# Kernel optimization log

Hardware: AMD Instinct MI355X
Metric: run time of the kernel (lower is better)

Reference implementation:

```python
import jax, jax.numpy as jnp
import numpy as np


def fps(xyz, npoint):
    # Farthest point sampling. xyz: [B, N, 3] -> idx [B, npoint] int32
    B, N, _ = xyz.shape
    d0 = jnp.full((B, N), 1e10, xyz.dtype)
    far0 = jnp.zeros((B,), jnp.int32)

    def step(carry, _):
        dist, far = carry
        centroid = jnp.take_along_axis(xyz, far[:, None, None], axis=1)  # [B,1,3]
        d = jnp.sum((xyz - centroid) ** 2, axis=-1)                      # [B,N]
        dist = jnp.minimum(dist, d)
        nxt = jnp.argmax(dist, axis=-1).astype(jnp.int32)
        return (dist, nxt), far

    _, idx = jax.lax.scan(step, (d0, far0), None, length=npoint)
    return idx.T  # [B, npoint]


def ball_query(radius, nsample, xyz, new_xyz):
    # xyz [B,N,3], new_xyz [B,S,3] -> idx [B,S,nsample] int32
    N = xyz.shape[1]
    sqr = (jnp.sum(new_xyz ** 2, -1)[:, :, None]
           + jnp.sum(xyz ** 2, -1)[:, None, :]
           - 2.0 * jnp.einsum('bsd,bnd->bsn', new_xyz, xyz))  # [B,S,N]
    idx = jnp.broadcast_to(jnp.arange(N, dtype=jnp.int32), sqr.shape)
    idx = jnp.where(sqr > radius * radius, N, idx)
    idx = jnp.sort(idx, axis=-1)[..., :nsample]
    first = idx[..., :1]  # centers are in xyz, so at least one in-radius index exists
    return jnp.where(idx == N, first, idx)


def _gather(x, idx):
    # x [B,N,C], idx [B,S,K] -> [B,S,K,C]
    return jax.vmap(lambda xb, ib: xb[ib])(x, idx)


def set_abstraction(xyz, points, npoint, radius, nsample, layers):
    # xyz [B,N,3]; points [B,N,D] or None; layers: list of (W [Co,Ci], b [Co])
    fps_idx = fps(xyz, npoint)                                   # [B,S]
    new_xyz = jnp.take_along_axis(xyz, fps_idx[..., None], axis=1)  # [B,S,3]
    idx = ball_query(radius, nsample, xyz, new_xyz)              # [B,S,K]
    grouped = _gather(xyz, idx) - new_xyz[:, :, None, :]         # [B,S,K,3] centered
    if points is not None:
        grouped = jnp.concatenate([grouped, _gather(points, idx)], axis=-1)
    feats = grouped  # [B,S,K,Cin]
    for W, b in layers:  # shared 1x1 conv MLP (BN folded, eval mode) + ReLU
        feats = jax.nn.relu(jnp.einsum('bskc,oc->bsko', feats, W) + b)
    new_points = jnp.max(feats, axis=2)  # max-pool over neighborhood -> [B,S,Cout]
    return new_xyz, new_points.transpose(0, 2, 1)  # [B,S,3], [B,Cout,S]


def setup_inputs() -> dict:
    key = jax.random.key(0)
    ks = jax.random.split(key, 13)
    xyz = jax.random.uniform(ks[0], (8, 6, 32768), dtype=jnp.float32)
    dims1 = [(64, 6), (64, 64), (128, 64)]
    dims2 = [(128, 131), (128, 128), (285, 128)]
    inp = {'xyz': xyz}
    i = 1
    for pre, dims in (('sa1', dims1), ('sa2', dims2)):
        for j, (o, c) in enumerate(dims, 1):
            inp[f'{pre}_w{j}'] = jax.random.normal(ks[i], (o, c), jnp.float32) * (1.0 / np.sqrt(c))
            inp[f'{pre}_b{j}'] = jax.random.normal(ks[i + 6], (o,), jnp.float32) * 0.05
            i += 1
    return inp


def reference(xyz, sa1_w1, sa1_b1, sa1_w2, sa1_b2, sa1_w3, sa1_b3,
              sa2_w1, sa2_b1, sa2_w2, sa2_b2, sa2_w3, sa2_b3):
    norm = xyz[:, 3:, :].transpose(0, 2, 1)   # [B,N,3]
    xyz3 = xyz[:, :3, :].transpose(0, 2, 1)   # [B,N,3]
    l1_xyz, l1_points = set_abstraction(
        xyz3, norm, 512, 0.025, 32,
        [(sa1_w1, sa1_b1), (sa1_w2, sa1_b2), (sa1_w3, sa1_b3)])
    l2_xyz, l2_points = set_abstraction(
        l1_xyz, l1_points.transpose(0, 2, 1), 256, 0.05, 64,
        [(sa2_w1, sa2_b1), (sa2_w2, sa2_b2), (sa2_w3, sa2_b3)])
    return l2_xyz.transpose(0, 2, 1), l2_points.transpose(0, 2, 1)  # [B,3,256],[B,256,285]
```

## Files before the change

### kernel.cpp

```cpp
#include <hip/hip_runtime.h>

#define N1 32768
#define NP1 512
#define NS1 32
#define N2 512
#define NP2 256
#define NS2 64
#define POISON 0xAAAAAAAAu

__device__ __forceinline__ float fadd(float a, float b){ return __fadd_rn(a,b); }
__device__ __forceinline__ float fmul(float a, float b){ return __fmul_rn(a,b); }
__device__ __forceinline__ float fsub(float a, float b){ return __fsub_rn(a,b); }

__device__ __forceinline__ float dist3(float px,float py,float pz,float cx,float cy,float cz){
    float dx = fsub(px,cx), dy = fsub(py,cy), dz = fsub(pz,cz);
    return fadd(fadd(fmul(dx,dx), fmul(dy,dy)), fmul(dz,dz));
}
__device__ __forceinline__ float sumsq3(float x,float y,float z){
    return fadd(fadd(fmul(x,x), fmul(y,y)), fmul(z,z));
}
__device__ __forceinline__ float dot3(float ax,float ay,float az,float bx,float by,float bz){
    return fadd(fadd(fmul(ax,bx), fmul(ay,by)), fmul(az,bz));
}

__device__ __forceinline__ unsigned long long shflmax64(unsigned long long k, int off){
    unsigned long long o = __shfl_xor(k, off, 64);
    return o > k ? o : k;
}

#define FPS1_M  16
#define ST1_X   (FPS1_M + NP1/4 + 1)

__global__ __launch_bounds__(256) void stage1_kernel(const float* __restrict__ xyz,
                                                     float* __restrict__ new_xyz1,
                                                     unsigned long long* __restrict__ bests,
                                                     int* __restrict__ idx1, float r2,
                                                     float* __restrict__ new_xyz2,
                                                     float* __restrict__ out0)
{
    const int x = blockIdx.x;
    const int b = blockIdx.y;
    const int t = threadIdx.x;
    const int lane = t & 63;
    const int wid  = t >> 6;
    const float* xb = xyz + (size_t)b * 6 * N1;

    if (x < FPS1_M) {
        const int m = x;
        __shared__ unsigned long long wb[4];
        __shared__ float cw[4];

        const int base = m * (N1 / FPS1_M);
        float px[8], py[8], pz[8], dd[8];
#pragma unroll
        for (int j = 0; j < 8; ++j) {
            int n = base + t + j * 256;
            px[j] = xb[n];
            py[j] = xb[N1 + n];
            pz[j] = xb[2*N1 + n];
            dd[j] = 1e10f;
        }

        float cx = xb[0], cy = xb[N1], cz = xb[2*N1];

        for (int s = 0; s < NP1; ++s) {
            if (m == 0 && t == 0) {
                unsigned* o = (unsigned*)(new_xyz1 + ((size_t)b*NP1 + s)*3);
                __hip_atomic_store(o+0, __float_as_uint(cx), __ATOMIC_RELAXED, __HIP_MEMORY_SCOPE_AGENT);
                __hip_atomic_store(o+1, __float_as_uint(cy), __ATOMIC_RELAXED, __HIP_MEMORY_SCOPE_AGENT);
                __hip_atomic_store(o+2, __float_as_uint(cz), __ATOMIC_RELAXED, __HIP_MEMORY_SCOPE_AGENT);
            }
            if (s == NP1 - 1) break;

            float bv = -1.0f; int bi = base + t;
#pragma unroll
            for (int j = 0; j < 8; ++j) {
                float d  = dist3(px[j],py[j],pz[j],cx,cy,cz);
                float nd = fminf(dd[j], d);
                dd[j] = nd;
                if (nd > bv) { bv = nd; bi = base + t + j*256; }
            }
            unsigned long long pk = ((unsigned long long)__float_as_uint(bv) << 15)
                                  | (unsigned long long)(32767 - bi);
            pk = shflmax64(pk, 1);  pk = shflmax64(pk, 2);  pk = shflmax64(pk, 4);
            pk = shflmax64(pk, 8);  pk = shflmax64(pk, 16); pk = shflmax64(pk, 32);
            if (lane == 0) wb[wid] = pk;
            __syncthreads();

            if (wid == 0) {
                unsigned long long k4 = (lane < 4) ? wb[lane] : 0ull;
                k4 = shflmax64(k4, 1); k4 = shflmax64(k4, 2);
                unsigned long long* slotPar = bests + ((size_t)b*2 + (s & 1))*FPS1_M;
                if (lane == 0)
                    __hip_atomic_store(slotPar + m, (k4 << 10) | (unsigned long long)s,
                                       __ATOMIC_RELAXED, __HIP_MEMORY_SCOPE_AGENT);
                unsigned long long myv = 0; bool done = (lane >= FPS1_M);
                float ccx = 0.f, ccy = 0.f, ccz = 0.f;
                while (__ballot(done) != 0xFFFFFFFFFFFFFFFFull) {
                    if (!done) {
                        unsigned long long v = __hip_atomic_load(slotPar + lane,
                                                 __ATOMIC_RELAXED, __HIP_MEMORY_SCOPE_AGENT);
                        if ((unsigned)(v & 1023ull) == (unsigned)s) {
                            done = true; myv = v;
                            int idx = 32767 - (int)((v >> 10) & 0x7fffull);
                            ccx = xb[idx]; ccy = xb[N1 + idx]; ccz = xb[2*N1 + idx];
                        }
                    }
                }
                unsigned long long w = myv;
                w = shflmax64(w, 1); w = shflmax64(w, 2); w = shflmax64(w, 4); w = shflmax64(w, 8);
                int wl = (int)__ffsll(__ballot(myv == w)) - 1;
                float ncx = __shfl(ccx, wl, 64);
                float ncy = __shfl(ccy, wl, 64);
                float ncz = __shfl(ccz, wl, 64);
                if (lane == 0) { cw[0] = ncx; cw[1] = ncy; cw[2] = ncz; }
            }
            __syncthreads();
            cx = cw[0]; cy = cw[1]; cz = cw[2];
        }
        return;
    }

    if (x < FPS1_M + NP1/4) {
        const int s = (x - FPS1_M)*4 + wid;
        unsigned ux = 0, uy = 0, uz = 0;
        if (lane == 0) {
            const unsigned* cp = (const unsigned*)(new_xyz1 + ((size_t)b*NP1 + s)*3);
            for (;;) {
                ux = __hip_atomic_load(cp+0, __ATOMIC_RELAXED, __HIP_MEMORY_SCOPE_AGENT);
                uy = __hip_atomic_load(cp+1, __ATOMIC_RELAXED, __HIP_MEMORY_SCOPE_AGENT);
                uz = __hip_atomic_load(cp+2, __ATOMIC_RELAXED, __HIP_MEMORY_SCOPE_AGENT);
                if (ux != POISON && uy != POISON && uz != POISON) break;
                __builtin_amdgcn_s_sleep(32);
            }
        }
        float cx = __uint_as_float(__shfl((int)ux, 0, 64));
        float cy = __uint_as_float(__shfl((int)uy, 0, 64));
        float cz = __uint_as_float(__shfl((int)uz, 0, 64));

        float snew = sumsq3(cx,cy,cz);
        int* out = idx1 + ((size_t)b*NP1 + s)*NS1;
        int cnt = 0, first = 0;
        for (int ch = 0; ch < N1/64; ++ch) {
            int n = ch*64 + lane;
            float px_ = xb[n], py_ = xb[N1+n], pz_ = xb[2*N1+n];
            float sx  = sumsq3(px_,py_,pz_);
            float dt  = dot3(cx,cy,cz,px_,py_,pz_);
            float sqr = fsub(fadd(snew, sx), fmul(2.0f, dt));
            bool inb = !(sqr > r2);
            unsigned long long mask = __ballot(inb);
            if (mask) {
                if (cnt == 0) first = ch*64 + (int)(__ffsll((unsigned long long)mask) - 1);
                if (inb) {
                    int pos = cnt + (int)__popcll(mask & ((1ull << lane) - 1ull));
                    if (pos < NS1) out[pos] = n;
                }
                cnt += (int)__popcll(mask);
                if (cnt >= NS1) break;
            }
        }
        int c = cnt < NS1 ? cnt : NS1;
        if (lane < NS1 && lane >= c) out[lane] = first;
        return;
    }

    {
        __shared__ float c3[N2*3];
        const float* src = new_xyz1 + (size_t)b*N2*3;
        for (int e = t; e < N2*3; e += 256) {
            const unsigned* sp = (const unsigned*)(src + e);
            unsigned v;
            for (;;) {
                v = __hip_atomic_load(sp, __ATOMIC_RELAXED, __HIP_MEMORY_SCOPE_AGENT);
                if (v != POISON) break;
                __builtin_amdgcn_s_sleep(32);
            }
            c3[e] = __uint_as_float(v);
        }
        __syncthreads();
        if (t >= 64) return;

        float px[8], py[8], pz[8], dd[8];
#pragma unroll
        for (int j = 0; j < 8; ++j) {
            int n = t + j*64;
            px[j] = c3[n*3]; py[j] = c3[n*3+1]; pz[j] = c3[n*3+2];
            dd[j] = 1e10f;
        }
        int cur = 0;
        for (int s = 0; s < NP2; ++s) {
            float cx = c3[cur*3], cy = c3[cur*3+1], cz = c3[cur*3+2];
            if (t == 0) {
                float* o = new_xyz2 + ((size_t)b*NP2 + s)*3;
                o[0]=cx; o[1]=cy; o[2]=cz;
                out0[b*3*NP2 + s]         = cx;
                out0[b*3*NP2 + NP2 + s]   = cy;
                out0[b*3*NP2 + 2*NP2 + s] = cz;
            }
            float bv = -1.0f; int bi = 0;
#pragma unroll
            for (int j = 0; j < 8; ++j) {
                float d  = dist3(px[j],py[j],pz[j],cx,cy,cz);
                float nd = fminf(dd[j], d);
                dd[j] = nd;
                int n = t + j*64;
                if (nd > bv) { bv = nd; bi = n; }
            }
            unsigned long long pk = ((unsigned long long)__float_as_uint(bv) << 9)
                                  | (unsigned long long)(511 - bi);
            pk = shflmax64(pk, 1);  pk = shflmax64(pk, 2);  pk = shflmax64(pk, 4);
            pk = shflmax64(pk, 8);  pk = shflmax64(pk, 16); pk = shflmax64(pk, 32);
            cur = 511 - (int)(pk & 511ull);
        }
    }
}

__global__ __launch_bounds__(256) void mlp1_ball2_kernel(const float* __restrict__ xyz,
    const float* __restrict__ new_xyz1, const int* __restrict__ idx1,
    const float* __restrict__ W1, const float* __restrict__ B1,
    const float* __restrict__ W2, const float* __restrict__ B2,
    const float* __restrict__ W3, const float* __restrict__ B3,
    float* __restrict__ l1_points,
    const float* __restrict__ new_xyz2, int* __restrict__ idx2, float r2b)
{
    const int b = blockIdx.y;
    const int t = threadIdx.x;

    if (blockIdx.x >= NP1) {
        if (t < 64) {
            const int s = blockIdx.x - NP1;
            const int lane = t;
            const float* pb = new_xyz1 + (size_t)b*N2*3;
            const float* cp = new_xyz2 + ((size_t)b*NP2 + s)*3;
            float cx = cp[0], cy = cp[1], cz = cp[2];
            float snew = sumsq3(cx,cy,cz);
            int* out = idx2 + ((size_t)b*NP2 + s)*NS2;
            int cnt = 0, first = 0;
            for (int ch = 0; ch < N2/64; ++ch) {
                int n = ch*64 + lane;
                float x = pb[n*3], y = pb[n*3+1], z = pb[n*3+2];
                float sx  = sumsq3(x,y,z);
                float dt  = dot3(cx,cy,cz,x,y,z);
                float sqr = fsub(fadd(snew, sx), fmul(2.0f, dt));
                bool inb = !(sqr > r2b);
                unsigned long long mask = __ballot(inb);
                if (mask) {
                    if (cnt == 0) first = ch*64 + (int)(__ffsll((unsigned long long)mask) - 1);
                    if (inb) {
                        int pos = cnt + (int)__popcll(mask & ((1ull << lane) - 1ull));
                        if (pos < NS2) out[pos] = n;
                    }
                    cnt += (int)__popcll(mask);
                    if (cnt >= NS2) break;
                }
            }
            int c = cnt < NS2 ? cnt : NS2;
            if (lane >= c) out[lane] = first;
        }
        return;
    }

    const int s = blockIdx.x;
    const float* xb = xyz + (size_t)b*6*N1;
    __shared__ __align__(16) float inb_[NS1][6];
    __shared__ __align__(16) float h1_[NS1][64];
    __shared__ __align__(16) float h2_[NS1][64];
    __shared__ __align__(16) float red_[2][128];
    __shared__ int sidx[NS1];

    const float* cp = new_xyz1 + ((size_t)b*NP1 + s)*3;
    float c0 = cp[0], c1 = cp[1], c2 = cp[2];
    if (t < NS1) sidx[t] = idx1[((size_t)b*NP1+s)*NS1 + t];
    __syncthreads();
    if (t < NS1*6) {
        int k = t / 6, c = t % 6;
        int n = sidx[k];
        float v = xb[(size_t)c*N1 + n];
        if (c == 0) v -= c0; else if (c == 1) v -= c1; else if (c == 2) v -= c2;
        inb_[k][c] = v;
    }
    __syncthreads();
    {
        int o = t & 63, kg = t >> 6;
        float w[6];
#pragma unroll
        for (int c = 0; c < 6; ++c) w[c] = W1[o*6+c];
        float bias = B1[o];
#pragma unroll
        for (int kk = 0; kk < 8; ++kk) {
            int k = kg*8 + kk;
            float a = 0.f;
#pragma unroll
            for (int c = 0; c < 6; ++c) a = fmaf(inb_[k][c], w[c], a);
            h1_[k][o] = fmaxf(a + bias, 0.f);
        }
    }
    __syncthreads();
    {
        int o = t & 63, kg = t >> 6;
        float acc[8] = {};
        for (int ch = 0; ch < 8; ++ch) {
            const float4 wa = *(const float4*)&W2[o*64 + ch*8];
            const float4 wbv = *(const float4*)&W2[o*64 + ch*8 + 4];
#pragma unroll
            for (int kk = 0; kk < 8; ++kk) {
                int k = kg*8+kk;
                const float4 a0 = *(const float4*)&h1_[k][ch*8];
                const float4 a1 = *(const float4*)&h1_[k][ch*8+4];
                acc[kk] = fmaf(a0.x, wa.x, acc[kk]);
                acc[kk] = fmaf(a0.y, wa.y, acc[kk]);
                acc[kk] = fmaf(a0.z, wa.z, acc[kk]);
                acc[kk] = fmaf(a0.w, wa.w, acc[kk]);
                acc[kk] = fmaf(a1.x, wbv.x, acc[kk]);
                acc[kk] = fmaf(a1.y, wbv.y, acc[kk]);
                acc[kk] = fmaf(a1.z, wbv.z, acc[kk]);
                acc[kk] = fmaf(a1.w, wbv.w, acc[kk]);
            }
        }
        float bias = B2[o];
#pragma unroll
        for (int kk = 0; kk < 8; ++kk) h2_[kg*8+kk][o] = fmaxf(acc[kk] + bias, 0.f);
    }
    __syncthreads();
    {
        int o = t & 127, kg = t >> 7;
        float acc[16] = {};
        for (int ch = 0; ch < 8; ++ch) {
            const float4 wa = *(const float4*)&W3[o*64 + ch*8];
            const float4 wbv = *(const float4*)&W3[o*64 + ch*8 + 4];
#pragma unroll
            for (int kk = 0; kk < 16; ++kk) {
                int k = kg*16+kk;
                const float4 a0 = *(const float4*)&h2_[k][ch*8];
                const float4 a1 = *(const float4*)&h2_[k][ch*8+4];
                acc[kk] = fmaf(a0.x, wa.x, acc[kk]);
                acc[kk] = fmaf(a0.y, wa.y, acc[kk]);
                acc[kk] = fmaf(a0.z, wa.z, acc[kk]);
                acc[kk] = fmaf(a0.w, wa.w, acc[kk]);
                acc[kk] = fmaf(a1.x, wbv.x, acc[kk]);
                acc[kk] = fmaf(a1.y, wbv.y, acc[kk]);
                acc[kk] = fmaf(a1.z, wbv.z, acc[kk]);
                acc[kk] = fmaf(a1.w, wbv.w, acc[kk]);
            }
        }
        float bias = B3[o];
        float m = -1e30f;
#pragma unroll
        for (int kk = 0; kk < 16; ++kk) m = fmaxf(m, fmaxf(acc[kk] + bias, 0.f));
        red_[kg][o] = m;
    }
    __syncthreads();
    if (t < 128) {
        float m = fmaxf(red_[0][t], red_[1][t]);
        l1_points[((size_t)b*NP1+s)*128 + t] = m;
    }
}

__global__ __launch_bounds__(256) void mlp2_kernel(
    const float* __restrict__ new_xyz1, const float* __restrict__ l1_points,
    const float* __restrict__ new_xyz2, const int* __restrict__ idx2,
    const float* __restrict__ W1, const float* __restrict__ B1,
    const float* __restrict__ W2, const float* __restrict__ B2,
    const float* __restrict__ W3, const float* __restrict__ B3,
    float* __restrict__ out1)
{
    const int s = blockIdx.x, b = blockIdx.y;
    const int t = threadIdx.x;
    __shared__ __align__(16) float inb_[32][132];
    __shared__ __align__(16) float h1_[32][128];
    __shared__ __align__(16) float h2_[32][128];
    __shared__ int sidx[NS2];

    const float* cp = new_xyz2 + ((size_t)b*NP2+s)*3;
    float c0=cp[0], c1=cp[1], c2=cp[2];
    if (t < NS2) sidx[t] = idx2[((size_t)b*NP2+s)*NS2 + t];

    const int o1 = t & 63, o2 = o1 + 64, g = t >> 6;
    float vmax0 = -1e30f, vmax1 = -1e30f;

    for (int half = 0; half < 2; ++half) {
        __syncthreads();
        for (int e = t; e < 32*32; e += 256) {
            int kk = e >> 5, c4 = e & 31;
            int n = sidx[half*32 + kk];
            *(float4*)&inb_[kk][c4*4] =
                *(const float4*)&l1_points[((size_t)b*N2 + n)*128 + c4*4];
        }
        for (int e = t; e < 32*3; e += 256) {
            int kk = e / 3, c = e % 3;
            int n = sidx[half*32 + kk];
            inb_[kk][128 + c] = new_xyz1[((size_t)b*N2 + n)*3 + c]
                              - (c==0 ? c0 : (c==1 ? c1 : c2));
        }
        __syncthreads();
        {
            float accA[8] = {}, accB[8] = {};
            for (int ch = 0; ch < 16; ++ch) {
                float wa[8], wbv[8];
#pragma unroll
                for (int j = 0; j < 8; ++j) {
                    wa[j]  = W1[o1*131 + 3 + ch*8 + j];
                    wbv[j] = W1[o2*131 + 3 + ch*8 + j];
                }
#pragma unroll
                for (int kk = 0; kk < 8; ++kk) {
                    int k = g*8 + kk;
                    const float4 a0 = *(const float4*)&inb_[k][ch*8];
                    const float4 a1 = *(const float4*)&inb_[k][ch*8+4];
                    accA[kk] = fmaf(a0.x, wa[0], accA[kk]);
                    accA[kk] = fmaf(a0.y, wa[1], accA[kk]);
                    accA[kk] = fmaf(a0.z, wa[2], accA[kk]);
                    accA[kk] = fmaf(a0.w, wa[3], accA[kk]);
                    accA[kk] = fmaf(a1.x, wa[4], accA[kk]);
                    accA[kk] = fmaf(a1.y, wa[5], accA[kk]);
                    accA[kk] = fmaf(a1.z, wa[6], accA[kk]);
                    accA[kk] = fmaf(a1.w, wa[7], accA[kk]);
                    accB[kk] = fmaf(a0.x, wbv[0], accB[kk]);
                    accB[kk] = fmaf(a0.y, wbv[1], accB[kk]);
                    accB[kk] = fmaf(a0.z, wbv[2], accB[kk]);
                    accB[kk] = fmaf(a0.w, wbv[3], accB[kk]);
                    accB[kk] = fmaf(a1.x, wbv[4], accB[kk]);
                    accB[kk] = fmaf(a1.y, wbv[5], accB[kk]);
                    accB[kk] = fmaf(a1.z, wbv[6], accB[kk]);
                    accB[kk] = fmaf(a1.w, wbv[7], accB[kk]);
                }
            }
            float ta0=W1[o1*131+0], ta1=W1[o1*131+1], ta2=W1[o1*131+2];
            float tb0=W1[o2*131+0], tb1=W1[o2*131+1], tb2=W1[o2*131+2];
            float biasA = B1[o1], biasB = B1[o2];
#pragma unroll
            for (int kk = 0; kk < 8; ++kk) {
                int k = g*8 + kk;
                float f0 = inb_[k][128], f1 = inb_[k][129], f2 = inb_[k][130];
                float vA = accA[kk];
                vA = fmaf(f0, ta0, vA); vA = fmaf(f1, ta1, vA); vA = fmaf(f2, ta2, vA);
                float vB = accB[kk];
                vB = fmaf(f0, tb0, vB); vB = fmaf(f1, tb1, vB); vB = fmaf(f2, tb2, vB);
                h1_[k][o1] = fmaxf(vA + biasA, 0.f);
                h1_[k][o2] = fmaxf(vB + biasB, 0.f);
            }
        }
        __syncthreads();
        {
            float accA[8] = {}, accB[8] = {};
            for (int ch = 0; ch < 16; ++ch) {
                const float4 wa0 = *(const float4*)&W2[o1*128 + ch*8];
                const float4 wa1 = *(const float4*)&W2[o1*128 + ch*8 + 4];
                const float4 wb0 = *(const float4*)&W2[o2*128 + ch*8];
                const float4 wb1 = *(const float4*)&W2[o2*128 + ch*8 + 4];
#pragma unroll
                for (int kk = 0; kk < 8; ++kk) {
                    int k = g*8 + kk;
                    const float4 a0 = *(const float4*)&h1_[k][ch*8];
                    const float4 a1 = *(const float4*)&h1_[k][ch*8+4];
                    accA[kk] = fmaf(a0.x, wa0.x, accA[kk]);
                    accA[kk] = fmaf(a0.y, wa0.y, accA[kk]);
                    accA[kk] = fmaf(a0.z, wa0.z, accA[kk]);
                    accA[kk] = fmaf(a0.w, wa0.w, accA[kk]);
                    accA[kk] = fmaf(a1.x, wa1.x, accA[kk]);
                    accA[kk] = fmaf(a1.y, wa1.y, accA[kk]);
                    accA[kk] = fmaf(a1.z, wa1.z, accA[kk]);
                    accA[kk] = fmaf(a1.w, wa1.w, accA[kk]);
                    accB[kk] = fmaf(a0.x, wb0.x, accB[kk]);
                    accB[kk] = fmaf(a0.y, wb0.y, accB[kk]);
                    accB[kk] = fmaf(a0.z, wb0.z, accB[kk]);
                    accB[kk] = fmaf(a0.w, wb0.w, accB[kk]);
                    accB[kk] = fmaf(a1.x, wb1.x, accB[kk]);
                    accB[kk] = fmaf(a1.y, wb1.y, accB[kk]);
                    accB[kk] = fmaf(a1.z, wb1.z, accB[kk]);
                    accB[kk] = fmaf(a1.w, wb1.w, accB[kk]);
                }
            }
            float biasA = B2[o1], biasB = B2[o2];
#pragma unroll
            for (int kk = 0; kk < 8; ++kk) {
                int k = g*8 + kk;
                h2_[k][o1] = fmaxf(accA[kk] + biasA, 0.f);
                h2_[k][o2] = fmaxf(accB[kk] + biasB, 0.f);
            }
        }
        __syncthreads();
        {
            {
                float acc[32] = {};
                for (int ch = 0; ch < 16; ++ch) {
                    const float4 w0 = *(const float4*)&W3[t*128 + ch*8];
                    const float4 w1 = *(const float4*)&W3[t*128 + ch*8 + 4];
#pragma unroll
                    for (int kk = 0; kk < 32; ++kk) {
                        const float4 a0 = *(const float4*)&h2_[kk][ch*8];
                        const float4 a1 = *(const float4*)&h2_[kk][ch*8+4];
                        acc[kk] = fmaf(a0.x, w0.x, acc[kk]);
                        acc[kk] = fmaf(a0.y, w0.y, acc[kk]);
                        acc[kk] = fmaf(a0.z, w0.z, acc[kk]);
                        acc[kk] = fmaf(a0.w, w0.w, acc[kk]);
                        acc[kk] = fmaf(a1.x, w1.x, acc[kk]);
                        acc[kk] = fmaf(a1.y, w1.y, acc[kk]);
                        acc[kk] = fmaf(a1.z, w1.z, acc[kk]);
                        acc[kk] = fmaf(a1.w, w1.w, acc[kk]);
                    }
                }
                float bias = B3[t];
                float mm = vmax0;
#pragma unroll
                for (int kk = 0; kk < 32; ++kk) mm = fmaxf(mm, fmaxf(acc[kk] + bias, 0.f));
                vmax0 = mm;
            }
            if (t < 29) {
                int o = t + 256;
                float acc[32] = {};
                for (int ch = 0; ch < 16; ++ch) {
                    const float4 w0 = *(const float4*)&W3[o*128 + ch*8];
                    const float4 w1 = *(const float4*)&W3[o*128 + ch*8 + 4];
#pragma unroll
                    for (int kk = 0; kk < 32; ++kk) {
                        const float4 a0 = *(const float4*)&h2_[kk][ch*8];
                        const float4 a1 = *(const float4*)&h2_[kk][ch*8+4];
                        acc[kk] = fmaf(a0.x, w0.x, acc[kk]);
                        acc[kk] = fmaf(a0.y, w0.y, acc[kk]);
                        acc[kk] = fmaf(a0.z, w0.z, acc[kk]);
                        acc[kk] = fmaf(a0.w, w0.w, acc[kk]);
                        acc[kk] = fmaf(a1.x, w1.x, acc[kk]);
                        acc[kk] = fmaf(a1.y, w1.y, acc[kk]);
                        acc[kk] = fmaf(a1.z, w1.z, acc[kk]);
                        acc[kk] = fmaf(a1.w, w1.w, acc[kk]);
                    }
                }
                float bias = B3[o];
                float mm = vmax1;
#pragma unroll
                for (int kk = 0; kk < 32; ++kk) mm = fmaxf(mm, fmaxf(acc[kk] + bias, 0.f));
                vmax1 = mm;
            }
        }
    }
    out1[((size_t)b*NP2+s)*285 + t] = vmax0;
    if (t < 29) out1[((size_t)b*NP2+s)*285 + t + 256] = vmax1;
}

extern "C" void kernel_launch(void* const* d_in, const int* in_sizes, int n_in,
                              void* d_out, int out_size, void* d_ws, size_t ws_size,
                              hipStream_t stream)
{
    (void)in_sizes; (void)n_in; (void)out_size; (void)ws_size;
    const float* xyz  = (const float*)d_in[0];
    const float* s1w1 = (const float*)d_in[1];  const float* s1b1 = (const float*)d_in[2];
    const float* s1w2 = (const float*)d_in[3];  const float* s1b2 = (const float*)d_in[4];
    const float* s1w3 = (const float*)d_in[5];  const float* s1b3 = (const float*)d_in[6];
    const float* s2w1 = (const float*)d_in[7];  const float* s2b1 = (const float*)d_in[8];
    const float* s2w2 = (const float*)d_in[9];  const float* s2b2 = (const float*)d_in[10];
    const float* s2w3 = (const float*)d_in[11]; const float* s2b3 = (const float*)d_in[12];

    float* ws        = (float*)d_ws;
    float* new_xyz1  = ws;
    float* new_xyz2  = ws + 12288;
    float* l1_points = ws + 18432;
    int*   idx1      = (int*)(ws + 542720);
    int*   idx2      = idx1 + 131072;
    unsigned long long* bests = (unsigned long long*)(ws + 804864);

    float* out0 = (float*)d_out;
    float* out1 = out0 + 8*3*256;

    const float r2a = (float)(0.025*0.025);
    const float r2b = (float)(0.05*0.05);

    stage1_kernel    <<<dim3(ST1_X, 8),   dim3(256), 0, stream>>>(xyz, new_xyz1, bests,
                         idx1, r2a, new_xyz2, out0);
    mlp1_ball2_kernel<<<dim3(NP1+NP2, 8), dim3(256), 0, stream>>>(xyz, new_xyz1, idx1,
                         s1w1,s1b1,s1w2,s1b2,s1w3,s1b3, l1_points,
                         new_xyz2, idx2, r2b);
    mlp2_kernel      <<<dim3(NP2, 8),     dim3(256), 0, stream>>>(new_xyz1, l1_points,
                         new_xyz2, idx2, s2w1,s2b1,s2w2,s2b2,s2w3,s2b3, out1);
}
```

Before: 1.792 ms.

## Merge all three stages into one persistent kernel with poison-flag dataflow

Combines the FPS, ball-query, MLP1, second-level FPS/ball-query and MLP2 kernels into a single launch. A linear block index assigns each block to a stage, and later stages spin-poll on poisoned workspace values that earlier stages publish with atomic stores. The aim is to overlap the MLP and second-level work with the long serial FPS and to remove inter-kernel launch gaps. The cost is larger shared memory per block, which can lower occupancy. Correctness now depends on producer blocks being scheduled before the consumers that poll them, so ordering or residency could cause stalls or deadlock.

New measurement: 1.700 ms. 1.05x faster.

```diff
diff --git a/kernel.cpp b/kernel.cpp
--- a/kernel.cpp
+++ b/kernel.cpp
@@ -22,34 +22,75 @@
 __device__ __forceinline__ float dot3(float ax,float ay,float az,float bx,float by,float bz){
     return fadd(fadd(fmul(ax,bx), fmul(ay,by)), fmul(az,bz));
 }
-
 __device__ __forceinline__ unsigned long long shflmax64(unsigned long long k, int off){
     unsigned long long o = __shfl_xor(k, off, 64);
     return o > k ? o : k;
 }
 
+__device__ __forceinline__ void astore_f(float* p, float v){
+    __hip_atomic_store((unsigned*)p, __float_as_uint(v), __ATOMIC_RELAXED, __HIP_MEMORY_SCOPE_AGENT);
+}
+__device__ __forceinline__ void astore_i(int* p, int v){
+    __hip_atomic_store((unsigned*)p, (unsigned)v, __ATOMIC_RELAXED, __HIP_MEMORY_SCOPE_AGENT);
+}
+template<int SLP>
+__device__ __forceinline__ float poll_f(const float* p){
+    unsigned v;
+    for(;;){
+        v = __hip_atomic_load((const unsigned*)p, __ATOMIC_RELAXED, __HIP_MEMORY_SCOPE_AGENT);
+        if (v != POISON) break;
+        __builtin_amdgcn_s_sleep(SLP);
+    }
+    return __uint_as_float(v);
+}
+template<int SLP>
+__device__ __forceinline__ int poll_i(const int* p){
+    unsigned v;
+    for(;;){
+        v = __hip_atomic_load((const unsigned*)p, __ATOMIC_RELAXED, __HIP_MEMORY_SCOPE_AGENT);
+        if (v != POISON) break;
+        __builtin_amdgcn_s_sleep(SLP);
+    }
+    return (int)v;
+}
+
 #define FPS1_M  16
-#define ST1_X   (FPS1_M + NP1/4 + 1)
-
-__global__ __launch_bounds__(256) void stage1_kernel(const float* __restrict__ xyz,
-                                                     float* __restrict__ new_xyz1,
-                                                     unsigned long long* __restrict__ bests,
-                                                     int* __restrict__ idx1, float r2,
-                                                     float* __restrict__ new_xyz2,
-                                                     float* __restrict__ out0)
+#define L_B1   128
+#define L_F2   1152
+#define L_M1   1160
+#define L_B2   5256
+#define L_M2   5768
+#define L_TOT  7816
+
+__global__ __launch_bounds__(256) void mega_kernel(const float* __restrict__ xyz,
+    float* __restrict__ new_xyz1, unsigned long long* __restrict__ bests,
+    int* __restrict__ idx1, float r2a,
+    float* __restrict__ new_xyz2, float* __restrict__ out0,
+    const float* __restrict__ M1W1, const float* __restrict__ M1B1,
+    const float* __restrict__ M1W2, const float* __restrict__ M1B2,
+    const float* __restrict__ M1W3, const float* __restrict__ M1B3,
+    float* __restrict__ l1_points,
+    int* __restrict__ idx2, float r2b,
+    const float* __restrict__ M2W1, const float* __restrict__ M2B1,
+    const float* __restrict__ M2W2, const float* __restrict__ M2B2,
+    const float* __restrict__ M2W3, const float* __restrict__ M2B3,
+    float* __restrict__ out1)
 {
-    const int x = blockIdx.x;
-    const int b = blockIdx.y;
+    const int l = blockIdx.x;
     const int t = threadIdx.x;
     const int lane = t & 63;
     const int wid  = t >> 6;
-    const float* xb = xyz + (size_t)b * 6 * N1;
-
-    if (x < FPS1_M) {
-        const int m = x;
-        __shared__ unsigned long long wb[4];
-        __shared__ float cw[4];
-
+
+    __shared__ unsigned long long wb[4];
+    __shared__ float cw[4];
+    __shared__ __align__(16) float ldsA[32*132];
+    __shared__ __align__(16) float ldsB[32*128];
+    __shared__ int sidx_sh[64];
+
+    if (l < L_B1) {
+        const int m = l & 15;
+        const int b = l >> 4;
+        const float* xb = xyz + (size_t)b * 6 * N1;
         const int base = m * (N1 / FPS1_M);
         float px[8], py[8], pz[8], dd[8];
 #pragma unroll
@@ -60,15 +101,12 @@
             pz[j] = xb[2*N1 + n];
             dd[j] = 1e10f;
         }
-
         float cx = xb[0], cy = xb[N1], cz = xb[2*N1];
 
         for (int s = 0; s < NP1; ++s) {
             if (m == 0 && t == 0) {
-                unsigned* o = (unsigned*)(new_xyz1 + ((size_t)b*NP1 + s)*3);
-                __hip_atomic_store(o+0, __float_as_uint(cx), __ATOMIC_RELAXED, __HIP_MEMORY_SCOPE_AGENT);
-                __hip_atomic_store(o+1, __float_as_uint(cy), __ATOMIC_RELAXED, __HIP_MEMORY_SCOPE_AGENT);
-                __hip_atomic_store(o+2, __float_as_uint(cz), __ATOMIC_RELAXED, __HIP_MEMORY_SCOPE_AGENT);
+                float* o = new_xyz1 + ((size_t)b*NP1 + s)*3;
+                astore_f(o+0, cx); astore_f(o+1, cy); astore_f(o+2, cz);
             }
             if (s == NP1 - 1) break;
 
@@ -121,62 +159,45 @@
         return;
     }
 
-    if (x < FPS1_M + NP1/4) {
-        const int s = (x - FPS1_M)*4 + wid;
-        unsigned ux = 0, uy = 0, uz = 0;
-        if (lane == 0) {
-            const unsigned* cp = (const unsigned*)(new_xyz1 + ((size_t)b*NP1 + s)*3);
-            for (;;) {
-                ux = __hip_atomic_load(cp+0, __ATOMIC_RELAXED, __HIP_MEMORY_SCOPE_AGENT);
-                uy = __hip_atomic_load(cp+1, __ATOMIC_RELAXED, __HIP_MEMORY_SCOPE_AGENT);
-                uz = __hip_atomic_load(cp+2, __ATOMIC_RELAXED, __HIP_MEMORY_SCOPE_AGENT);
-                if (ux != POISON && uy != POISON && uz != POISON) break;
-                __builtin_amdgcn_s_sleep(32);
-            }
-        }
-        float cx = __uint_as_float(__shfl((int)ux, 0, 64));
-        float cy = __uint_as_float(__shfl((int)uy, 0, 64));
-        float cz = __uint_as_float(__shfl((int)uz, 0, 64));
+    if (l < L_F2) {
+        const int i = l - L_B1;
+        const int b = i >> 7;
+        const int s = (i & 127)*4 + wid;
+        const float* xb = xyz + (size_t)b*6*N1;
+        const float* cp = new_xyz1 + ((size_t)b*NP1 + s)*3;
+        float cx = poll_f<32>(cp+0), cy = poll_f<32>(cp+1), cz = poll_f<32>(cp+2);
 
         float snew = sumsq3(cx,cy,cz);
         int* out = idx1 + ((size_t)b*NP1 + s)*NS1;
         int cnt = 0, first = 0;
         for (int ch = 0; ch < N1/64; ++ch) {
             int n = ch*64 + lane;
-            float px_ = xb[n], py_ = xb[N1+n], pz_ = xb[2*N1+n];
-            float sx  = sumsq3(px_,py_,pz_);
-            float dt  = dot3(cx,cy,cz,px_,py_,pz_);
+            float x = xb[n], y = xb[N1+n], z = xb[2*N1+n];
+            float sx  = sumsq3(x,y,z);
+            float dt  = dot3(cx,cy,cz,x,y,z);
             float sqr = fsub(fadd(snew, sx), fmul(2.0f, dt));
-            bool inb = !(sqr > r2);
+            bool inb = !(sqr > r2a);
             unsigned long long mask = __ballot(inb);
             if (mask) {
                 if (cnt == 0) first = ch*64 + (int)(__ffsll((unsigned long long)mask) - 1);
                 if (inb) {
                     int pos = cnt + (int)__popcll(mask & ((1ull << lane) - 1ull));
-                    if (pos < NS1) out[pos] = n;
+                    if (pos < NS1) astore_i(out + pos, n);
                 }
                 cnt += (int)__popcll(mask);
                 if (cnt >= NS1) break;
             }
         }
         int c = cnt < NS1 ? cnt : NS1;
-        if (lane < NS1 && lane >= c) out[lane] = first;
+        if (lane < NS1 && lane >= c) astore_i(out + lane, first);
         return;
     }
 
-    {
-        __shared__ float c3[N2*3];
+    if (l < L_M1) {
+        const int b = l - L_F2;
+        float* c3 = ldsA;
         const float* src = new_xyz1 + (size_t)b*N2*3;
-        for (int e = t; e < N2*3; e += 256) {
-            const unsigned* sp = (const unsigned*)(src + e);
-            unsigned v;
-            for (;;) {
-                v = __hip_atomic_load(sp, __ATOMIC_RELAXED, __HIP_MEMORY_SCOPE_AGENT);
-                if (v != POISON) break;
-                __builtin_amdgcn_s_sleep(32);
-            }
-            c3[e] = __uint_as_float(v);
-        }
+        for (int e = t; e < N2*3; e += 256) c3[e] = poll_f<32>(src + e);
         __syncthreads();
         if (t >= 64) return;
 
@@ -192,7 +213,7 @@
             float cx = c3[cur*3], cy = c3[cur*3+1], cz = c3[cur*3+2];
             if (t == 0) {
                 float* o = new_xyz2 + ((size_t)b*NP2 + s)*3;
-                o[0]=cx; o[1]=cy; o[2]=cz;
+                astore_f(o+0, cx); astore_f(o+1, cy); astore_f(o+2, cz);
                 out0[b*3*NP2 + s]         = cx;
                 out0[b*3*NP2 + NP2 + s]   = cy;
                 out0[b*3*NP2 + 2*NP2 + s] = cz;
@@ -212,330 +233,314 @@
             pk = shflmax64(pk, 8);  pk = shflmax64(pk, 16); pk = shflmax64(pk, 32);
             cur = 511 - (int)(pk & 511ull);
         }
-    }
-}
-
-__global__ __launch_bounds__(256) void mlp1_ball2_kernel(const float* __restrict__ xyz,
-    const float* __restrict__ new_xyz1, const int* __restrict__ idx1,
-    const float* __restrict__ W1, const float* __restrict__ B1,
-    const float* __restrict__ W2, const float* __restrict__ B2,
-    const float* __restrict__ W3, const float* __restrict__ B3,
-    float* __restrict__ l1_points,
-    const float* __restrict__ new_xyz2, int* __restrict__ idx2, float r2b)
-{
-    const int b = blockIdx.y;
-    const int t = threadIdx.x;
-
-    if (blockIdx.x >= NP1) {
-        if (t < 64) {
-            const int s = blockIdx.x - NP1;
-            const int lane = t;
-            const float* pb = new_xyz1 + (size_t)b*N2*3;
-            const float* cp = new_xyz2 + ((size_t)b*NP2 + s)*3;
-            float cx = cp[0], cy = cp[1], cz = cp[2];
-            float snew = sumsq3(cx,cy,cz);
-            int* out = idx2 + ((size_t)b*NP2 + s)*NS2;
-            int cnt = 0, first = 0;
-            for (int ch = 0; ch < N2/64; ++ch) {
-                int n = ch*64 + lane;
-                float x = pb[n*3], y = pb[n*3+1], z = pb[n*3+2];
-                float sx  = sumsq3(x,y,z);
-                float dt  = dot3(cx,cy,cz,x,y,z);
-                float sqr = fsub(fadd(snew, sx), fmul(2.0f, dt));
-                bool inb = !(sqr > r2b);
-                unsigned long long mask = __ballot(inb);
-                if (mask) {
-                    if (cnt == 0) first = ch*64 + (int)(__ffsll((unsigned long long)mask) - 1);
-                    if (inb) {
-                        int pos = cnt + (int)__popcll(mask & ((1ull << lane) - 1ull));
-                        if (pos < NS2) out[pos] = n;
-                    }
-                    cnt += (int)__popcll(mask);
-                    if (cnt >= NS2) break;
-                }
-            }
-            int c = cnt < NS2 ? cnt : NS2;
-            if (lane >= c) out[lane] = first;
-        }
         return;
     }
 
-    const int s = blockIdx.x;
-    const float* xb = xyz + (size_t)b*6*N1;
-    __shared__ __align__(16) float inb_[NS1][6];
-    __shared__ __align__(16) float h1_[NS1][64];
-    __shared__ __align__(16) float h2_[NS1][64];
-    __shared__ __align__(16) float red_[2][128];
-    __shared__ int sidx[NS1];
-
-    const float* cp = new_xyz1 + ((size_t)b*NP1 + s)*3;
-    float c0 = cp[0], c1 = cp[1], c2 = cp[2];
-    if (t < NS1) sidx[t] = idx1[((size_t)b*NP1+s)*NS1 + t];
-    __syncthreads();
-    if (t < NS1*6) {
-        int k = t / 6, c = t % 6;
-        int n = sidx[k];
-        float v = xb[(size_t)c*N1 + n];
-        if (c == 0) v -= c0; else if (c == 1) v -= c1; else if (c == 2) v -= c2;
-        inb_[k][c] = v;
-    }
-    __syncthreads();
-    {
-        int o = t & 63, kg = t >> 6;
-        float w[6];
-#pragma unroll
-        for (int c = 0; c < 6; ++c) w[c] = W1[o*6+c];
-        float bias = B1[o];
-#pragma unroll
-        for (int kk = 0; kk < 8; ++kk) {
-            int k = kg*8 + kk;
-            float a = 0.f;
-#pragma unroll
-            for (int c = 0; c < 6; ++c) a = fmaf(inb_[k][c], w[c], a);
-            h1_[k][o] = fmaxf(a + bias, 0.f);
-        }
-    }
-    __syncthreads();
-    {
-        int o = t & 63, kg = t >> 6;
-        float acc[8] = {};
-        for (int ch = 0; ch < 8; ++ch) {
-            const float4 wa = *(const float4*)&W2[o*64 + ch*8];
-            const float4 wbv = *(const float4*)&W2[o*64 + ch*8 + 4];
-#pragma unroll
-            for (int kk = 0; kk < 8; ++kk) {
-                int k = kg*8+kk;
-                const float4 a0 = *(const float4*)&h1_[k][ch*8];
-                const float4 a1 = *(const float4*)&h1_[k][ch*8+4];
-                acc[kk] = fmaf(a0.x, wa.x, acc[kk]);
-                acc[kk] = fmaf(a0.y, wa.y, acc[kk]);
-                acc[kk] = fmaf(a0.z, wa.z, acc[kk]);
-                acc[kk] = fmaf(a0.w, wa.w, acc[kk]);
-                acc[kk] = fmaf(a1.x, wbv.x, acc[kk]);
-                acc[kk] = fmaf(a1.y, wbv.y, acc[kk]);
-                acc[kk] = fmaf(a1.z, wbv.z, acc[kk]);
-                acc[kk] = fmaf(a1.w, wbv.w, acc[kk]);
-            }
-        }
-        float bias = B2[o];
-#pragma unroll
-        for (int kk = 0; kk < 8; ++kk) h2_[kg*8+kk][o] = fmaxf(acc[kk] + bias, 0.f);
-    }
-    __syncthreads();
-    {
-        int o = t & 127, kg = t >> 7;
-        float acc[16] = {};
-        for (int ch = 0; ch < 8; ++ch) {
-            const float4 wa = *(const float4*)&W3[o*64 + ch*8];
-            const float4 wbv = *(const float4*)&W3[o*64 + ch*8 + 4];
-#pragma unroll
-            for (int kk = 0; kk < 16; ++kk) {
-                int k = kg*16+kk;
-                const float4 a0 = *(const float4*)&h2_[k][ch*8];
-                const float4 a1 = *(const float4*)&h2_[k][ch*8+4];
-                acc[kk] = fmaf(a0.x, wa.x, acc[kk]);
-                acc[kk] = fmaf(a0.y, wa.y, acc[kk]);
-                acc[kk] = fmaf(a0.z, wa.z, acc[kk]);
-                acc[kk] = fmaf(a0.w, wa.w, acc[kk]);
-                acc[kk] = fmaf(a1.x, wbv.x, acc[kk]);
-                acc[kk] = fmaf(a1.y, wbv.y, acc[kk]);
-                acc[kk] = fmaf(a1.z, wbv.z, acc[kk]);
-                acc[kk] = fmaf(a1.w, wbv.w, acc[kk]);
-            }
-        }
-        float bias = B3[o];
-        float m = -1e30f;
-#pragma unroll
-        for (int kk = 0; kk < 16; ++kk) m = fmaxf(m, fmaxf(acc[kk] + bias, 0.f));
-        red_[kg][o] = m;
-    }
-    __syncthreads();
-    if (t < 128) {
-        float m = fmaxf(red_[0][t], red_[1][t]);
-        l1_points[((size_t)b*NP1+s)*128 + t] = m;
-    }
-}
-
-__global__ __launch_bounds__(256) void mlp2_kernel(
-    const float* __restrict__ new_xyz1, const float* __restrict__ l1_points,
-    const float* __restrict__ new_xyz2, const int* __restrict__ idx2,
-    const float* __restrict__ W1, const float* __restrict__ B1,
-    const float* __restrict__ W2, const float* __restrict__ B2,
-    const float* __restrict__ W3, const float* __restrict__ B3,
-    float* __restrict__ out1)
-{
-    const int s = blockIdx.x, b = blockIdx.y;
-    const int t = threadIdx.x;
-    __shared__ __align__(16) float inb_[32][132];
-    __shared__ __align__(16) float h1_[32][128];
-    __shared__ __align__(16) float h2_[32][128];
-    __shared__ int sidx[NS2];
-
-    const float* cp = new_xyz2 + ((size_t)b*NP2+s)*3;
-    float c0=cp[0], c1=cp[1], c2=cp[2];
-    if (t < NS2) sidx[t] = idx2[((size_t)b*NP2+s)*NS2 + t];
-
-    const int o1 = t & 63, o2 = o1 + 64, g = t >> 6;
-    float vmax0 = -1e30f, vmax1 = -1e30f;
-
-    for (int half = 0; half < 2; ++half) {
+    if (l < L_B2) {
+        const int i = l - L_M1;
+        const int b = i >> 9;
+        const int s = i & 511;
+        const float* xb = xyz + (size_t)b*6*N1;
+        float (*inb6)[6]   = (float(*)[6])ldsA;
+        float (*h1m)[64]   = (float(*)[64])(ldsA + 192);
+        float (*h2m)[64]   = (float(*)[64])ldsB;
+        float (*redm)[128] = (float(*)[128])(ldsB + 2048);
+
+        const float* cp = new_xyz1 + ((size_t)b*NP1 + s)*3;
+        float c0 = poll_f<32>(cp+0), c1 = poll_f<32>(cp+1), c2 = poll_f<32>(cp+2);
+        if (t < NS1) sidx_sh[t] = poll_i<32>(idx1 + ((size_t)b*NP1+s)*NS1 + t);
         __syncthreads();
-        for (int e = t; e < 32*32; e += 256) {
-            int kk = e >> 5, c4 = e & 31;
-            int n = sidx[half*32 + kk];
-            *(float4*)&inb_[kk][c4*4] =
-                *(const float4*)&l1_points[((size_t)b*N2 + n)*128 + c4*4];
-        }
-        for (int e = t; e < 32*3; e += 256) {
-            int kk = e / 3, c = e % 3;
-            int n = sidx[half*32 + kk];
-            inb_[kk][128 + c] = new_xyz1[((size_t)b*N2 + n)*3 + c]
-                              - (c==0 ? c0 : (c==1 ? c1 : c2));
+        if (t < NS1*6) {
+            int k = t / 6, c = t % 6;
+            int n = sidx_sh[k];
+            float v = xb[(size_t)c*N1 + n];
+            if (c == 0) v -= c0; else if (c == 1) v -= c1; else if (c == 2) v -= c2;
+            inb6[k][c] = v;
         }
         __syncthreads();
         {
-            float accA[8] = {}, accB[8] = {};
-            for (int ch = 0; ch < 16; ++ch) {
-                float wa[8], wbv[8];
-#pragma unroll
-                for (int j = 0; j < 8; ++j) {
-                    wa[j]  = W1[o1*131 + 3 + ch*8 + j];
-                    wbv[j] = W1[o2*131 + 3 + ch*8 + j];
-                }
+            int o = t & 63, kg = t >> 6;
+            float w[6];
+#pragma unroll
+            for (int c = 0; c < 6; ++c) w[c] = M1W1[o*6+c];
+            float bias = M1B1[o];
+#pragma unroll
+            for (int kk = 0; kk < 8; ++kk) {
+                int k = kg*8 + kk;
+                float a = 0.f;
+#pragma unroll
+                for (int c = 0; c < 6; ++c) a = fmaf(inb6[k][c], w[c], a);
+                h1m[k][o] = fmaxf(a + bias, 0.f);
+            }
+        }
+        __syncthreads();
+        {
+            int o = t & 63, kg = t >> 6;
+            float acc[8] = {};
+            for (int ch = 0; ch < 8; ++ch) {
+                const float4 wa = *(const float4*)&M1W2[o*64 + ch*8];
+                const float4 wbv = *(const float4*)&M1W2[o*64 + ch*8 + 4];
+#pragma unroll
+                for (int kk = 0; kk < 8; ++kk) {
+                    int k = kg*8+kk;
+                    const float4 a0 = *(const float4*)&h1m[k][ch*8];
+                    const float4 a1 = *(const float4*)&h1m[k][ch*8+4];
+                    acc[kk] = fmaf(a0.x, wa.x, acc[kk]);
+                    acc[kk] = fmaf(a0.y, wa.y, acc[kk]);
+                    acc[kk] = fmaf(a0.z, wa.z, acc[kk]);
+                    acc[kk] = fmaf(a0.w, wa.w, acc[kk]);
+                    acc[kk] = fmaf(a1.x, wbv.x, acc[kk]);
+                    acc[kk] = fmaf(a1.y, wbv.y, acc[kk]);
+                    acc[kk] = fmaf(a1.z, wbv.z, acc[kk]);
+                    acc[kk] = fmaf(a1.w, wbv.w, acc[kk]);
+                }
+            }
+            float bias = M1B2[o];
+#pragma unroll
+            for (int kk = 0; kk < 8; ++kk) h2m[kg*8+kk][o] = fmaxf(acc[kk] + bias, 0.f);
+        }
+        __syncthreads();
+        {
+            int o = t & 127, kg = t >> 7;
+            float acc[16] = {};
+            for (int ch = 0; ch < 8; ++ch) {
+                const float4 wa = *(const float4*)&M1W3[o*64 + ch*8];
+                const float4 wbv = *(const float4*)&M1W3[o*64 + ch*8 + 4];
+#pragma unroll
+                for (int kk = 0; kk < 16; ++kk) {
+                    int k = kg*16+kk;
+                    const float4 a0 = *(const float4*)&h2m[k][ch*8];
+                    const float4 a1 = *(const float4*)&h2m[k][ch*8+4];
+                    acc[kk] = fmaf(a0.x, wa.x, acc[kk]);
+                    acc[kk] = fmaf(a0.y, wa.y, acc[kk]);
+                    acc[kk] = fmaf(a0.z, wa.z, acc[kk]);
+                    acc[kk] = fmaf(a0.w, wa.w, acc[kk]);
+                    acc[kk] = fmaf(a1.x, wbv.x, acc[kk]);
+                    acc[kk] = fmaf(a1.y, wbv.y, acc[kk]);
+                    acc[kk] = fmaf(a1.z, wbv.z, acc[kk]);
+                    acc[kk] = fmaf(a1.w, wbv.w, acc[kk]);
+                }
+            }
+            float bias = M1B3[o];
+            float m = -1e30f;
+#pragma unroll
+            for (int kk = 0; kk < 16; ++kk) m = fmaxf(m, fmaxf(acc[kk] + bias, 0.f));
+            redm[kg][o] = m;
+        }
+        __syncthreads();
+        if (t < 128) {
+            float m = fmaxf(redm[0][t], redm[1][t]);
+            astore_f(l1_points + ((size_t)b*NP1+s)*128 + t, m);
+        }
+        return;
+    }
+
+    if (l < L_M2) {
+        const int i = l - L_B2;
+        const int b = i >> 6;
+        const int s = (i & 63)*4 + wid;
+        const float* pb = new_xyz1 + (size_t)b*N2*3;
+        const float* cp = new_xyz2 + ((size_t)b*NP2 + s)*3;
+        float cx = poll_f<32>(cp+0), cy = poll_f<32>(cp+1), cz = poll_f<32>(cp+2);
+        float snew = sumsq3(cx,cy,cz);
+        int* out = idx2 + ((size_t)b*NP2 + s)*NS2;
+        int cnt = 0, first = 0;
+        for (int ch = 0; ch < N2/64; ++ch) {
+            int n = ch*64 + lane;
+            float x = poll_f<8>(&pb[n*3]), y = poll_f<8>(&pb[n*3+1]), z = poll_f<8>(&pb[n*3+2]);
+            float sx  = sumsq3(x,y,z);
+            float dt  = dot3(cx,cy,cz,x,y,z);
+            float sqr = fsub(fadd(snew, sx), fmul(2.0f, dt));
+            bool inb = !(sqr > r2b);
+            unsigned long long mask = __ballot(inb);
+            if (mask) {
+                if (cnt == 0) first = ch*64 + (int)(__ffsll((unsigned long long)mask) - 1);
+                if (inb) {
+                    int pos = cnt + (int)__popcll(mask & ((1ull << lane) - 1ull));
+                    if (pos < NS2) astore_i(out + pos, n);
+                }
+                cnt += (int)__popcll(mask);
+                if (cnt >= NS2) break;
+            }
+        }
+        int c = cnt < NS2 ? cnt : NS2;
+        if (lane >= c) astore_i(out + lane, first);
+        return;
+    }
+
+    {
+        const int i = l - L_M2;
+        const int b = i >> 8;
+        const int s = i & 255;
+        float (*inb2)[132] = (float(*)[132])ldsA;
+        float (*h1_)[128]  = (float(*)[128])ldsB;
+        float (*h2_)[128]  = (float(*)[128])ldsA;
+
+        const float* cp = new_xyz2 + ((size_t)b*NP2+s)*3;
+        float c0 = poll_f<32>(cp+0), c1 = poll_f<32>(cp+1), c2 = poll_f<32>(cp+2);
+        if (t < NS2) sidx_sh[t] = poll_i<32>(idx2 + ((size_t)b*NP2+s)*NS2 + t);
+
+        const int o1 = t & 63, o2 = o1 + 64, g = t >> 6;
+        float vmax0 = -1e30f, vmax1 = -1e30f;
+
+        for (int half = 0; half < 2; ++half) {
+            __syncthreads();
+            for (int e = t; e < 32*128; e += 256) {
+                int kk = e >> 7, c = e & 127;
+                int n = sidx_sh[half*32 + kk];
+                inb2[kk][c] = poll_f<8>(l1_points + ((size_t)b*N2 + n)*128 + c);
+            }
+            for (int e = t; e < 32*3; e += 256) {
+                int kk = e / 3, c = e % 3;
+                int n = sidx_sh[half*32 + kk];
+                inb2[kk][128 + c] = poll_f<8>(new_xyz1 + ((size_t)b*N2 + n)*3 + c)
+                                  - (c==0 ? c0 : (c==1 ? c1 : c2));
+            }
+            __syncthreads();
+            {
+                float accA[8] = {}, accB[8] = {};
+                for (int ch = 0; ch < 16; ++ch) {
+                    float wa[8], wbv[8];
+#pragma unroll
+                    for (int j = 0; j < 8; ++j) {
+                        wa[j]  = M2W1[o1*131 + 3 + ch*8 + j];
+                        wbv[j] = M2W1[o2*131 + 3 + ch*8 + j];
+                    }
+#pragma unroll
+                    for (int kk = 0; kk < 8; ++kk) {
+                        int k = g*8 + kk;
+                        const float4 a0 = *(const float4*)&inb2[k][ch*8];
+                        const float4 a1 = *(const float4*)&inb2[k][ch*8+4];
+                        accA[kk] = fmaf(a0.x, wa[0], accA[kk]);
+                        accA[kk] = fmaf(a0.y, wa[1], accA[kk]);
+                        accA[kk] = fmaf(a0.z, wa[2], accA[kk]);
+                        accA[kk] = fmaf(a0.w, wa[3], accA[kk]);
+                        accA[kk] = fmaf(a1.x, wa[4], accA[kk]);
+                        accA[kk] = fmaf(a1.y, wa[5], accA[kk]);
+                        accA[kk] = fmaf(a1.z, wa[6], accA[kk]);
+                        accA[kk] = fmaf(a1.w, wa[7], accA[kk]);
+                        accB[kk] = fmaf(a0.x, wbv[0], accB[kk]);
+                        accB[kk] = fmaf(a0.y, wbv[1], accB[kk]);
+                        accB[kk] = fmaf(a0.z, wbv[2], accB[kk]);
+                        accB[kk] = fmaf(a0.w, wbv[3], accB[kk]);
+                        accB[kk] = fmaf(a1.x, wbv[4], accB[kk]);
+                        accB[kk] = fmaf(a1.y, wbv[5], accB[kk]);
+                        accB[kk] = fmaf(a1.z, wbv[6], accB[kk]);
+                        accB[kk] = fmaf(a1.w, wbv[7], accB[kk]);
+                    }
+                }
+                float ta0=M2W1[o1*131+0], ta1=M2W1[o1*131+1], ta2=M2W1[o1*131+2];
+                float tb0=M2W1[o2*131+0], tb1=M2W1[o2*131+1], tb2=M2W1[o2*131+2];
+                float biasA = M2B1[o1], biasB = M2B1[o2];
 #pragma unroll
                 for (int kk = 0; kk < 8; ++kk) {
                     int k = g*8 + kk;
-                    const float4 a0 = *(const float4*)&inb_[k][ch*8];
-                    const float4 a1 = *(const float4*)&inb_[k][ch*8+4];
-                    accA[kk] = fmaf(a0.x, wa[0], accA[kk]);
-                    accA[kk] = fmaf(a0.y, wa[1], accA[kk]);
-                    accA[kk] = fmaf(a0.z, wa[2], accA[kk]);
-                    accA[kk] = fmaf(a0.w, wa[3], accA[kk]);
-                    accA[kk] = fmaf(a1.x, wa[4], accA[kk]);
-                    accA[kk] = fmaf(a1.y, wa[5], accA[kk]);
-                    accA[kk] = fmaf(a1.z, wa[6], accA[kk]);
-                    accA[kk] = fmaf(a1.w, wa[7], accA[kk]);
-                    accB[kk] = fmaf(a0.x, wbv[0], accB[kk]);
-                    accB[kk] = fmaf(a0.y, wbv[1], accB[kk]);
-                    accB[kk] = fmaf(a0.z, wbv[2], accB[kk]);
-                    accB[kk] = fmaf(a0.w, wbv[3], accB[kk]);
-                    accB[kk] = fmaf(a1.x, wbv[4], accB[kk]);
-                    accB[kk] = fmaf(a1.y, wbv[5], accB[kk]);
-                    accB[kk] = fmaf(a1.z, wbv[6], accB[kk]);
-                    accB[kk] = fmaf(a1.w, wbv[7], accB[kk]);
-                }
-            }
-            float ta0=W1[o1*131+0], ta1=W1[o1*131+1], ta2=W1[o1*131+2];
-            float tb0=W1[o2*131+0], tb1=W1[o2*131+1], tb2=W1[o2*131+2];
-            float biasA = B1[o1], biasB = B1[o2];
-#pragma unroll
-            for (int kk = 0; kk < 8; ++kk) {
-                int k = g*8 + kk;
-                float f0 = inb_[k][128], f1 = inb_[k][129], f2 = inb_[k][130];
-                float vA = accA[kk];
-                vA = fmaf(f0, ta0, vA); vA = fmaf(f1, ta1, vA); vA = fmaf(f2, ta2, vA);
-                float vB = accB[kk];
-                vB = fmaf(f0, tb0, vB); vB = fmaf(f1, tb1, vB); vB = fmaf(f2, tb2, vB);
-                h1_[k][o1] = fmaxf(vA + biasA, 0.f);
-                h1_[k][o2] = fmaxf(vB + biasB, 0.f);
-            }
-        }
-        __syncthreads();
-        {
-            float accA[8] = {}, accB[8] = {};
-            for (int ch = 0; ch < 16; ++ch) {
-                const float4 wa0 = *(const float4*)&W2[o1*128 + ch*8];
-                const float4 wa1 = *(const float4*)&W2[o1*128 + ch*8 + 4];
-                const float4 wb0 = *(const float4*)&W2[o2*128 + ch*8];
-                const float4 wb1 = *(const float4*)&W2[o2*128 + ch*8 + 4];
+                    float f0 = inb2[k][128], f1 = inb2[k][129], f2 = inb2[k][130];
+                    float vA = accA[kk];
+                    vA = fmaf(f0, ta0, vA); vA = fmaf(f1, ta1, vA); vA = fmaf(f2, ta2, vA);
+                    float vB = accB[kk];
+                    vB = fmaf(f0, tb0, vB); vB = fmaf(f1, tb1, vB); vB = fmaf(f2, tb2, vB);
+                    h1_[k][o1] = fmaxf(vA + biasA, 0.f);
+                    h1_[k][o2] = fmaxf(vB + biasB, 0.f);
+                }
+            }
+            __syncthreads();
+            {
+                float accA[8] = {}, accB[8] = {};
+                for (int ch = 0; ch < 16; ++ch) {
+                    const float4 wa0 = *(const float4*)&M2W2[o1*128 + ch*8];
+                    const float4 wa1 = *(const float4*)&M2W2[o1*128 + ch*8 + 4];
+                    const float4 wb0 = *(const float4*)&M2W2[o2*128 + ch*8];
+                    const float4 wb1 = *(const float4*)&M2W2[o2*128 + ch*8 + 4];
+#pragma unroll
+                    for (int kk = 0; kk < 8; ++kk) {
+                        int k = g*8 + kk;
+                        const float4 a0 = *(const float4*)&h1_[k][ch*8];
+                        const float4 a1 = *(const float4*)&h1_[k][ch*8+4];
+                        accA[kk] = fmaf(a0.x, wa0.x, accA[kk]);
+                        accA[kk] = fmaf(a0.y, wa0.y, accA[kk]);
+                        accA[kk] = fmaf(a0.z, wa0.z, accA[kk]);
+                        accA[kk] = fmaf(a0.w, wa0.w, accA[kk]);
+                        accA[kk] = fmaf(a1.x, wa1.x, accA[kk]);
+                        accA[kk] = fmaf(a1.y, wa1.y, accA[kk]);
+                        accA[kk] = fmaf(a1.z, wa1.z, accA[kk]);
+                        accA[kk] = fmaf(a1.w, wa1.w, accA[kk]);
+                        accB[kk] = fmaf(a0.x, wb0.x, accB[kk]);
+                        accB[kk] = fmaf(a0.y, wb0.y, accB[kk]);
+                        accB[kk] = fmaf(a0.z, wb0.z, accB[kk]);
+                        accB[kk] = fmaf(a0.w, wb0.w, accB[kk]);
+                        accB[kk] = fmaf(a1.x, wb1.x, accB[kk]);
+                        accB[kk] = fmaf(a1.y, wb1.y, accB[kk]);
+                        accB[kk] = fmaf(a1.z, wb1.z, accB[kk]);
+                        accB[kk] = fmaf(a1.w, wb1.w, accB[kk]);
+                    }
+                }
+                float biasA = M2B2[o1], biasB = M2B2[o2];
 #pragma unroll
                 for (int kk = 0; kk < 8; ++kk) {
                     int k = g*8 + kk;
-                    const float4 a0 = *(const float4*)&h1_[k][ch*8];
-                    const float4 a1 = *(const float4*)&h1_[k][ch*8+4];
-                    accA[kk] = fmaf(a0.x, wa0.x, accA[kk]);
-                    accA[kk] = fmaf(a0.y, wa0.y, accA[kk]);
-                    accA[kk] = fmaf(a0.z, wa0.z, accA[kk]);
-                    accA[kk] = fmaf(a0.w, wa0.w, accA[kk]);
-                    accA[kk] = fmaf(a1.x, wa1.x, accA[kk]);
-                    accA[kk] = fmaf(a1.y, wa1.y, accA[kk]);
-                    accA[kk] = fmaf(a1.z, wa1.z, accA[kk]);
-                    accA[kk] = fmaf(a1.w, wa1.w, accA[kk]);
-                    accB[kk] = fmaf(a0.x, wb0.x, accB[kk]);
-                    accB[kk] = fmaf(a0.y, wb0.y, accB[kk]);
-                    accB[kk] = fmaf(a0.z, wb0.z, accB[kk]);
-                    accB[kk] = fmaf(a0.w, wb0.w, accB[kk]);
-                    accB[kk] = fmaf(a1.x, wb1.x, accB[kk]);
-                    accB[kk] = fmaf(a1.y, wb1.y, accB[kk]);
-                    accB[kk] = fmaf(a1.z, wb1.z, accB[kk]);
-                    accB[kk] = fmaf(a1.w, wb1.w, accB[kk]);
-                }
-            }
-            float biasA = B2[o1], biasB = B2[o2];
-#pragma unroll
-            for (int kk = 0; kk < 8; ++kk) {
-                int k = g*8 + kk;
-                h2_[k][o1] = fmaxf(accA[kk] + biasA, 0.f);
-                h2_[k][o2] = fmaxf(accB[kk] + biasB, 0.f);
-            }
-        }
-        __syncthreads();
-        {
+                    h2_[k][o1] = fmaxf(accA[kk] + biasA, 0.f);
+                    h2_[k][o2] = fmaxf(accB[kk] + biasB, 0.f);
+                }
+            }
+            __syncthreads();
             {
-                float acc[32] = {};
-                for (int ch = 0; ch < 16; ++ch) {
-                    const float4 w0 = *(const float4*)&W3[t*128 + ch*8];
-                    const float4 w1 = *(const float4*)&W3[t*128 + ch*8 + 4];
-#pragma unroll
-                    for (int kk = 0; kk < 32; ++kk) {
-                        const float4 a0 = *(const float4*)&h2_[kk][ch*8];
-                        const float4 a1 = *(const float4*)&h2_[kk][ch*8+4];
-                        acc[kk] = fmaf(a0.x, w0.x, acc[kk]);
-                        acc[kk] = fmaf(a0.y, w0.y, acc[kk]);
-                        acc[kk] = fmaf(a0.z, w0.z, acc[kk]);
-                        acc[kk] = fmaf(a0.w, w0.w, acc[kk]);
-                        acc[kk] = fmaf(a1.x, w1.x, acc[kk]);
-                        acc[kk] = fmaf(a1.y, w1.y, acc[kk]);
-                        acc[kk] = fmaf(a1.z, w1.z, acc[kk]);
-                        acc[kk] = fmaf(a1.w, w1.w, acc[kk]);
+                {
+                    float acc[32] = {};
+                    for (int ch = 0; ch < 16; ++ch) {
+                        const float4 w0 = *(const float4*)&M2W3[t*128 + ch*8];
+                        const float4 w1 = *(const float4*)&M2W3[t*128 + ch*8 + 4];
+#pragma unroll
+                        for (int kk = 0; kk < 32; ++kk) {
+                            const float4 a0 = *(const float4*)&h2_[kk][ch*8];
+                            const float4 a1 = *(const float4*)&h2_[kk][ch*8+4];
+                            acc[kk] = fmaf(a0.x, w0.x, acc[kk]);
+                            acc[kk] = fmaf(a0.y, w0.y, acc[kk]);
+                            acc[kk] = fmaf(a0.z, w0.z, acc[kk]);
+                            acc[kk] = fmaf(a0.w, w0.w, acc[kk]);
+                            acc[kk] = fmaf(a1.x, w1.x, acc[kk]);
+                            acc[kk] = fmaf(a1.y, w1.y, acc[kk]);
+                            acc[kk] = fmaf(a1.z, w1.z, acc[kk]);
+                            acc[kk] = fmaf(a1.w, w1.w, acc[kk]);
+                        }
                     }
-                }
-                float bias = B3[t];
-                float mm = vmax0;
-#pragma unroll
-                for (int kk = 0; kk < 32; ++kk) mm = fmaxf(mm, fmaxf(acc[kk] + bias, 0.f));
-                vmax0 = mm;
-            }
-            if (t < 29) {
-                int o = t + 256;
-                float acc[32] = {};
-                for (int ch = 0; ch < 16; ++ch) {
-                    const float4 w0 = *(const float4*)&W3[o*128 + ch*8];
-                    const float4 w1 = *(const float4*)&W3[o*128 + ch*8 + 4];
-#pragma unroll
-                    for (int kk = 0; kk < 32; ++kk) {
-                        const float4 a0 = *(const float4*)&h2_[kk][ch*8];
-                        const float4 a1 = *(const float4*)&h2_[kk][ch*8+4];
-                        acc[kk] = fmaf(a0.x, w0.x, acc[kk]);
-                        acc[kk] = fmaf(a0.y, w0.y, acc[kk]);
-                        acc[kk] = fmaf(a0.z, w0.z, acc[kk]);
-                        acc[kk] = fmaf(a0.w, w0.w, acc[kk]);
-                        acc[kk] = fmaf(a1.x, w1.x, acc[kk]);
-                        acc[kk] = fmaf(a1.y, w1.y, acc[kk]);
-                        acc[kk] = fmaf(a1.z, w1.z, acc[kk]);
-                        acc[kk] = fmaf(a1.w, w1.w, acc[kk]);
+                    float bias = M2B3[t];
+                    float mm = vmax0;
+#pragma unroll
+                    for (int kk = 0; kk < 32; ++kk) mm = fmaxf(mm, fmaxf(acc[kk] + bias, 0.f));
+                    vmax0 = mm;
+                }
+                if (t < 29) {
+                    int o = t + 256;
+                    float acc[32] = {};
+                    for (int ch = 0; ch < 16; ++ch) {
+                        const float4 w0 = *(const float4*)&M2W3[o*128 + ch*8];
+                        const float4 w1 = *(const float4*)&M2W3[o*128 + ch*8 + 4];
+#pragma unroll
+                        for (int kk = 0; kk < 32; ++kk) {
+                            const float4 a0 = *(const float4*)&h2_[kk][ch*8];
+                            const float4 a1 = *(const float4*)&h2_[kk][ch*8+4];
+                            acc[kk] = fmaf(a0.x, w0.x, acc[kk]);
+                            acc[kk] = fmaf(a0.y, w0.y, acc[kk]);
+                            acc[kk] = fmaf(a0.z, w0.z, acc[kk]);
+                            acc[kk] = fmaf(a0.w, w0.w, acc[kk]);
+                            acc[kk] = fmaf(a1.x, w1.x, acc[kk]);
+                            acc[kk] = fmaf(a1.y, w1.y, acc[kk]);
+                            acc[kk] = fmaf(a1.z, w1.z, acc[kk]);
+                            acc[kk] = fmaf(a1.w, w1.w, acc[kk]);
+                        }
                     }
-                }
-                float bias = B3[o];
-                float mm = vmax1;
-#pragma unroll
-                for (int kk = 0; kk < 32; ++kk) mm = fmaxf(mm, fmaxf(acc[kk] + bias, 0.f));
-                vmax1 = mm;
-            }
-        }
-    }
-    out1[((size_t)b*NP2+s)*285 + t] = vmax0;
-    if (t < 29) out1[((size_t)b*NP2+s)*285 + t + 256] = vmax1;
+                    float bias = M2B3[o];
+                    float mm = vmax1;
+#pragma unroll
+                    for (int kk = 0; kk < 32; ++kk) mm = fmaxf(mm, fmaxf(acc[kk] + bias, 0.f));
+                    vmax1 = mm;
+                }
+            }
+        }
+        out1[((size_t)b*NP2+s)*285 + t] = vmax0;
+        if (t < 29) out1[((size_t)b*NP2+s)*285 + t + 256] = vmax1;
+    }
 }
 
 extern "C" void kernel_launch(void* const* d_in, const int* in_sizes, int n_in,
@@ -565,11 +570,9 @@
     const float r2a = (float)(0.025*0.025);
     const float r2b = (float)(0.05*0.05);
 
-    stage1_kernel    <<<dim3(ST1_X, 8),   dim3(256), 0, stream>>>(xyz, new_xyz1, bests,
-                         idx1, r2a, new_xyz2, out0);
-    mlp1_ball2_kernel<<<dim3(NP1+NP2, 8), dim3(256), 0, stream>>>(xyz, new_xyz1, idx1,
-                         s1w1,s1b1,s1w2,s1b2,s1w3,s1b3, l1_points,
-                         new_xyz2, idx2, r2b);
-    mlp2_kernel      <<<dim3(NP2, 8),     dim3(256), 0, stream>>>(new_xyz1, l1_points,
-                         new_xyz2, idx2, s2w1,s2b1,s2w2,s2b2,s2w3,s2b3, out1);
-}
+    mega_kernel<<<dim3(L_TOT), dim3(256), 0, stream>>>(xyz,
+        new_xyz1, bests, idx1, r2a, new_xyz2, out0,
+        s1w1,s1b1,s1w2,s1b2,s1w3,s1b3, l1_points,
+        idx2, r2b,
+        s2w1,s2b1,s2w2,s2b2,s2w3,s2b3, out1);
+}
```
